# Optimization experiments

Hardware: AMD Instinct MI355X
Metric: run time of the kernel (lower is better)

The kernel has to match this reference:

```python
import jax, jax.numpy as jnp
import numpy as np

B = 16384            # number of subgraphs in the batch
NODES_PER_G = 50     # nodes per subgraph
N = B * NODES_PER_G  # total nodes = 819200
L = 3                # num_gcn_layers
EMB = 32             # emb_dim -> repr dim = (1+L)*EMB = 128
REPR = (1 + L) * EMB
PFEAT, FEAT = 1280, 200
P, D, I = 2000, 10000, 20000
RELS = 2


def setup_inputs() -> dict:
    key = jax.random.key(0)
    ks = jax.random.split(key, 16)
    node_repr = jax.random.normal(ks[0], (N, REPR), jnp.float32)
    profeat = jax.random.normal(ks[1], (P, PFEAT), jnp.float32)
    drugfeat = jax.random.normal(ks[2], (D, FEAT), jnp.float32)
    s1p = 1.0 / np.sqrt(PFEAT); s2 = 1.0 / np.sqrt(EMB); s1 = 1.0 / np.sqrt(FEAT)
    W1p = jax.random.normal(ks[3], (PFEAT, EMB), jnp.float32) * s1p
    b1p = jnp.zeros((EMB,), jnp.float32)
    W2p = jax.random.normal(ks[4], (EMB, EMB), jnp.float32) * s2
    b2p = jnp.zeros((EMB,), jnp.float32)
    W1 = jax.random.normal(ks[5], (FEAT, EMB), jnp.float32) * s1
    b1 = jnp.zeros((EMB,), jnp.float32)
    W2 = jax.random.normal(ks[6], (EMB, EMB), jnp.float32) * s2
    b2 = jnp.zeros((EMB,), jnp.float32)
    fc_in = 3 * REPR + 2 * EMB  # 448
    fc_W = jax.random.normal(ks[7], (fc_in, RELS), jnp.float32) / np.sqrt(fc_in)
    fc_b = jnp.zeros((RELS,), jnp.float32)
    # batched-graph structure: contiguous blocks of NODES_PER_G nodes per graph
    graph_ids = (jnp.arange(N, dtype=jnp.int32) // NODES_PER_G).astype(jnp.int32)
    # exactly one head (id==1) and one tail (id==2) node per graph -> their indices
    head_ids = (jnp.arange(B, dtype=jnp.int32) * NODES_PER_G)
    tail_ids = head_ids + 1
    node_idx = jax.random.randint(ks[8], (N,), 0, I, jnp.int32)
    proind = jax.random.randint(ks[9], (I,), 0, P, jnp.int32)
    drugind = jax.random.randint(ks[10], (I,), 0, D, jnp.int32)
    return dict(node_repr=node_repr, profeat=profeat, drugfeat=drugfeat,
                W1p=W1p, b1p=b1p, W2p=W2p, b2p=b2p,
                W1=W1, b1=b1, W2=W2, b2=b2, fc_W=fc_W, fc_b=fc_b,
                graph_ids=graph_ids, head_ids=head_ids, tail_ids=tail_ids,
                node_idx=node_idx, proind=proind, drugind=drugind)


def reference(node_repr, profeat, drugfeat, W1p, b1p, W2p, b2p,
              W1, b1, W2, b2, fc_W, fc_b,
              graph_ids, head_ids, tail_ids, node_idx, proind, drugind):
    # mean_nodes(g, 'repr'): per-graph mean pooling of node reprs
    sums = jax.ops.segment_sum(node_repr, graph_ids, num_segments=B)      # [B, REPR]
    cnts = jax.ops.segment_sum(jnp.ones((node_repr.shape[0],), node_repr.dtype),
                               graph_ids, num_segments=B)                # [B]
    g_out = sums / cnts[:, None]
    # head/tail embedding gathers (id==1 / id==2 nodes)
    head_embs = node_repr[head_ids]                                       # [B, REPR]
    tail_embs = node_repr[tail_ids]                                       # [B, REPR]
    # nested table lookups: profeat[proind[idx[head]]], drugfeat[drugind[idx[tail]]]
    head_feat = profeat[proind[node_idx[head_ids]]]                       # [B, PFEAT]
    tail_feat = drugfeat[drugind[node_idx[tail_ids]]]                     # [B, FEAT]
    # small fuse MLPs (dropout is identity in eval)
    fuse1 = jax.nn.relu(head_feat @ W1p + b1p) @ W2p + b2p                # [B, EMB]
    fuse2 = jax.nn.relu(tail_feat @ W1 + b1) @ W2 + b2                    # [B, EMB]
    g_rep = jnp.concatenate([g_out, head_embs, tail_embs, fuse1, fuse2], axis=1)
    return g_rep @ fc_W + fc_b                                            # [B, RELS]
```

## Files before the change

### kernel.cpp

```cpp
#include <hip/hip_runtime.h>
#include <hip/hip_bf16.h>

#define B_GRAPHS 16384
#define NODES_PER_G 50
#define REPR 128
#define PFEAT 1280
#define FEAT 200
#define EMB 32
#define P_ROWS 2000
#define D_ROWS 10000

#define NPF (P_ROWS / 8)
#define NDF (D_ROWS / 8)
#define NFUSE (NPF + NDF)
#define NPOOL (B_GRAPHS / 8)
#define NTOT (NPOOL + NFUSE)


__global__ __launch_bounds__(256) void merged_kernel(
    const float* __restrict__ nr,
    const float* __restrict__ profeat,
    const float* __restrict__ drugfeat,
    const float* __restrict__ W1p,
    const float* __restrict__ b1p,
    const float* __restrict__ W2p,
    const float* __restrict__ W1,
    const float* __restrict__ b1,
    const float* __restrict__ W2,
    const float* __restrict__ fcW,
    const float* __restrict__ b2p,
    const float* __restrict__ b2,
    float*       __restrict__ f1out,
    float*       __restrict__ f2out,
    float*       __restrict__ out)
{
    const int grp  = threadIdx.x >> 5;
    const int lane = threadIdx.x & 31;
    const int bid  = blockIdx.x;

    const int Fb  = (int)(((long)bid * NFUSE) / NTOT);
    const int Fb1 = (int)(((long)(bid + 1) * NFUSE) / NTOT);

    if (Fb1 == Fb) {
        const int g = (bid - Fb) * 8 + grp;
        const float4* nr4 = (const float4*)nr;
        const long base4 = (long)g * (NODES_PER_G * REPR / 4);

        float4 head4 = nr4[base4 + 0 * 32 + lane];
        float4 tail4 = nr4[base4 + 1 * 32 + lane];
        float4 s0, s1;
        s0.x = s0.y = s0.z = s0.w = 0.f;
        s1.x = s1.y = s1.z = s1.w = 0.f;
        #pragma unroll 8
        for (int i = 2; i < NODES_PER_G; i += 2) {
            float4 fa = nr4[base4 + i * 32 + lane];
            float4 fb = nr4[base4 + (i + 1) * 32 + lane];
            s0.x += fa.x; s0.y += fa.y; s0.z += fa.z; s0.w += fa.w;
            s1.x += fb.x; s1.y += fb.y; s1.z += fb.z; s1.w += fb.w;
        }
        float4 pool;
        pool.x = head4.x + tail4.x + s0.x + s1.x;
        pool.y = head4.y + tail4.y + s0.y + s1.y;
        pool.z = head4.z + tail4.z + s0.z + s1.z;
        pool.w = head4.w + tail4.w + s0.w + s1.w;

        const float4* fcW4 = (const float4*)fcW;
        float4 wg0 = fcW4[lane * 2 + 0],       wg1 = fcW4[lane * 2 + 1];
        float4 wh0 = fcW4[64 + lane * 2 + 0],  wh1 = fcW4[64 + lane * 2 + 1];
        float4 wt0 = fcW4[128 + lane * 2 + 0], wt1 = fcW4[128 + lane * 2 + 1];

        const float inv50 = 1.0f / (float)NODES_PER_G;
        float p0 = inv50 * (pool.x * wg0.x + pool.y * wg0.z + pool.z * wg1.x + pool.w * wg1.z)
                 + head4.x * wh0.x + head4.y * wh0.z + head4.z * wh1.x + head4.w * wh1.z
                 + tail4.x * wt0.x + tail4.y * wt0.z + tail4.z * wt1.x + tail4.w * wt1.z;
        float p1 = inv50 * (pool.x * wg0.y + pool.y * wg0.w + pool.z * wg1.y + pool.w * wg1.w)
                 + head4.x * wh0.y + head4.y * wh0.w + head4.z * wh1.y + head4.w * wh1.w
                 + tail4.x * wt0.y + tail4.y * wt0.w + tail4.z * wt1.y + tail4.w * wt1.w;

        {
            float2 fw1 = *(const float2*)(fcW + (384 + lane) * 2);
            float2 fw2 = *(const float2*)(fcW + (416 + lane) * 2);
            float bb1 = b2p[lane], bb2 = b2[lane];
            p0 = fmaf(bb1, fw1.x, fmaf(bb2, fw2.x, p0));
            p1 = fmaf(bb1, fw1.y, fmaf(bb2, fw2.y, p1));
        }

        for (int m = 16; m >= 1; m >>= 1) {
            p0 += __shfl_xor(p0, m, 32);
            p1 += __shfl_xor(p1, m, 32);
        }
        if (lane == 0) {
            out[g * 2 + 0] = p0;
            out[g * 2 + 1] = p1;
        }
    } else if (Fb < NPF) {
        const int p = Fb * 8 + grp;
        float m0 = 0.f, m1 = 0.f;
        #pragma unroll
        for (int k = 0; k < 32; ++k) {
            float w = W2p[lane * 32 + k];
            float2 fw = *(const float2*)(fcW + (384 + k) * 2);
            m0 = fmaf(w, fw.x, m0);
            m1 = fmaf(w, fw.y, m1);
        }
        const float4* pf4 = (const float4*)(profeat + (long)p * PFEAT);
        float a0 = 0.f, a1 = 0.f, a2 = 0.f, a3 = 0.f;
        #pragma unroll 4
        for (int q = 0; q < PFEAT / 4; q += 4) {
            float4 f0 = pf4[q], f1 = pf4[q + 1], f2 = pf4[q + 2], f3 = pf4[q + 3];
            int k = q * 4;
            a0 = fmaf(f0.x, W1p[(k + 0) * 32 + lane], a0);
            a0 = fmaf(f0.y, W1p[(k + 1) * 32 + lane], a0);
            a0 = fmaf(f0.z, W1p[(k + 2) * 32 + lane], a0);
            a0 = fmaf(f0.w, W1p[(k + 3) * 32 + lane], a0);
            a1 = fmaf(f1.x, W1p[(k + 4) * 32 + lane], a1);
            a1 = fmaf(f1.y, W1p[(k + 5) * 32 + lane], a1);
            a1 = fmaf(f1.z, W1p[(k + 6) * 32 + lane], a1);
            a1 = fmaf(f1.w, W1p[(k + 7) * 32 + lane], a1);
            a2 = fmaf(f2.x, W1p[(k + 8) * 32 + lane], a2);
            a2 = fmaf(f2.y, W1p[(k + 9) * 32 + lane], a2);
            a2 = fmaf(f2.z, W1p[(k + 10) * 32 + lane], a2);
            a2 = fmaf(f2.w, W1p[(k + 11) * 32 + lane], a2);
            a3 = fmaf(f3.x, W1p[(k + 12) * 32 + lane], a3);
            a3 = fmaf(f3.y, W1p[(k + 13) * 32 + lane], a3);
            a3 = fmaf(f3.z, W1p[(k + 14) * 32 + lane], a3);
            a3 = fmaf(f3.w, W1p[(k + 15) * 32 + lane], a3);
        }
        float h = fmaxf((a0 + a1) + (a2 + a3) + b1p[lane], 0.f);
        float p0 = h * m0, p1 = h * m1;
        for (int m = 16; m >= 1; m >>= 1) {
            p0 += __shfl_xor(p0, m, 32);
            p1 += __shfl_xor(p1, m, 32);
        }
        if (lane == 0) {
            f1out[p * 2 + 0] = p0;
            f1out[p * 2 + 1] = p1;
        }
    } else {
        const int d = (Fb - NPF) * 8 + grp;
        float m0 = 0.f, m1 = 0.f;
        #pragma unroll
        for (int k = 0; k < 32; ++k) {
            float w = W2[lane * 32 + k];
            float2 fw = *(const float2*)(fcW + (416 + k) * 2);
            m0 = fmaf(w, fw.x, m0);
            m1 = fmaf(w, fw.y, m1);
        }
        const float4* df4 = (const float4*)(drugfeat + (long)d * FEAT);
        float a0 = 0.f, a1 = 0.f;
        #pragma unroll 5
        for (int q = 0; q < FEAT / 4; q += 2) {
            float4 f0 = df4[q], f1 = df4[q + 1];
            int k = q * 4;
            a0 = fmaf(f0.x, W1[(k + 0) * 32 + lane], a0);
            a0 = fmaf(f0.y, W1[(k + 1) * 32 + lane], a0);
            a0 = fmaf(f0.z, W1[(k + 2) * 32 + lane], a0);
            a0 = fmaf(f0.w, W1[(k + 3) * 32 + lane], a0);
            a1 = fmaf(f1.x, W1[(k + 4) * 32 + lane], a1);
            a1 = fmaf(f1.y, W1[(k + 5) * 32 + lane], a1);
            a1 = fmaf(f1.z, W1[(k + 6) * 32 + lane], a1);
            a1 = fmaf(f1.w, W1[(k + 7) * 32 + lane], a1);
        }
        float h = fmaxf(a0 + a1 + b1[lane], 0.f);
        float p0 = h * m0, p1 = h * m1;
        for (int m = 16; m >= 1; m >>= 1) {
            p0 += __shfl_xor(p0, m, 32);
            p1 += __shfl_xor(p1, m, 32);
        }
        if (lane == 0) {
            f2out[d * 2 + 0] = p0;
            f2out[d * 2 + 1] = p1;
        }
    }
}

__global__ __launch_bounds__(256) void finalize_kernel(
    const int*   __restrict__ head_ids,
    const int*   __restrict__ tail_ids,
    const int*   __restrict__ node_idx,
    const int*   __restrict__ proind,
    const int*   __restrict__ drugind,
    const float* __restrict__ f1out,
    const float* __restrict__ f2out,
    const float* __restrict__ fcb,
    float*       __restrict__ out)
{
    const int g = blockIdx.x * 256 + threadIdx.x;
    if (g >= B_GRAPHS) return;
    const int prow = proind[node_idx[head_ids[g]]];
    const int drow = drugind[node_idx[tail_ids[g]]];
    const float2 f1v = *(const float2*)(f1out + prow * 2);
    const float2 f2v = *(const float2*)(f2out + drow * 2);
    float2 o = *(float2*)(out + g * 2);
    o.x += f1v.x + f2v.x + fcb[0];
    o.y += f1v.y + f2v.y + fcb[1];
    *(float2*)(out + g * 2) = o;
}

extern "C" void kernel_launch(void* const* d_in, const int* in_sizes, int n_in,
                              void* d_out, int out_size, void* d_ws, size_t ws_size,
                              hipStream_t stream) {
    const float* node_repr = (const float*)d_in[0];
    const float* profeat   = (const float*)d_in[1];
    const float* drugfeat  = (const float*)d_in[2];
    const float* W1p       = (const float*)d_in[3];
    const float* b1p       = (const float*)d_in[4];
    const float* W2p       = (const float*)d_in[5];
    const float* b2p       = (const float*)d_in[6];
    const float* W1        = (const float*)d_in[7];
    const float* b1        = (const float*)d_in[8];
    const float* W2        = (const float*)d_in[9];
    const float* b2        = (const float*)d_in[10];
    const float* fc_W      = (const float*)d_in[11];
    const float* fc_b      = (const float*)d_in[12];
    const int* head_ids    = (const int*)d_in[14];
    const int* tail_ids    = (const int*)d_in[15];
    const int* node_idx    = (const int*)d_in[16];
    const int* proind      = (const int*)d_in[17];
    const int* drugind     = (const int*)d_in[18];

    float* f1out = (float*)d_ws;
    float* f2out = (float*)d_ws + 2 * P_ROWS;
    float* out   = (float*)d_out;

    hipLaunchKernelGGL(merged_kernel, dim3(NTOT), dim3(256), 0, stream,
                       node_repr, profeat, drugfeat, W1p, b1p, W2p, W1, b1, W2,
                       fc_W, b2p, b2, f1out, f2out, out);

    hipLaunchKernelGGL(finalize_kernel, dim3(B_GRAPHS / 256), dim3(256), 0, stream,
                       head_ids, tail_ids, node_idx, proind, drugind,
                       f1out, f2out, fc_b, out);
}
```

Before: 107.3 us.

## Use one full 64-lane wavefront per graph in pooling branch

The pooling branch now assigns a whole 64-lane wavefront to each graph instead of a 32-lane half. Each lane reads two node rows per step, so the 50-node sum takes 25 loads split across four accumulators rather than 48 sequential loads over two. Head and tail rows are split across the two halves of the wavefront, and the bias terms go with them. Launch bounds now request 8 blocks per CU, which caps register use. The trade-off is twice as many pooling blocks and a longer shuffle reduction.

After: 133.3 us. 1.24x slower.

```diff
diff --git a/kernel.cpp b/kernel.cpp
--- a/kernel.cpp
+++ b/kernel.cpp
@@ -13,11 +13,11 @@
 #define NPF (P_ROWS / 8)
 #define NDF (D_ROWS / 8)
 #define NFUSE (NPF + NDF)
-#define NPOOL (B_GRAPHS / 8)
+#define NPOOL (B_GRAPHS / 4)
 #define NTOT (NPOOL + NFUSE)
 
 
-__global__ __launch_bounds__(256) void merged_kernel(
+__global__ __launch_bounds__(256, 8) void merged_kernel(
     const float* __restrict__ nr,
     const float* __restrict__ profeat,
     const float* __restrict__ drugfeat,
@@ -34,66 +34,78 @@
     float*       __restrict__ f2out,
     float*       __restrict__ out)
 {
-    const int grp  = threadIdx.x >> 5;
-    const int lane = threadIdx.x & 31;
     const int bid  = blockIdx.x;
-
     const int Fb  = (int)(((long)bid * NFUSE) / NTOT);
     const int Fb1 = (int)(((long)(bid + 1) * NFUSE) / NTOT);
 
     if (Fb1 == Fb) {
-        const int g = (bid - Fb) * 8 + grp;
+        const int wid = threadIdx.x >> 6;
+        const int l   = threadIdx.x & 63;
+        const int col = l & 31;
+        const int g   = (bid - Fb) * 4 + wid;
+
         const float4* nr4 = (const float4*)nr;
         const long base4 = (long)g * (NODES_PER_G * REPR / 4);
 
-        float4 head4 = nr4[base4 + 0 * 32 + lane];
-        float4 tail4 = nr4[base4 + 1 * 32 + lane];
-        float4 s0, s1;
-        s0.x = s0.y = s0.z = s0.w = 0.f;
-        s1.x = s1.y = s1.z = s1.w = 0.f;
-        #pragma unroll 8
-        for (int i = 2; i < NODES_PER_G; i += 2) {
-            float4 fa = nr4[base4 + i * 32 + lane];
-            float4 fb = nr4[base4 + (i + 1) * 32 + lane];
-            s0.x += fa.x; s0.y += fa.y; s0.z += fa.z; s0.w += fa.w;
-            s1.x += fb.x; s1.y += fb.y; s1.z += fb.z; s1.w += fb.w;
+        float4 sp = nr4[base4 + l];
+        float4 a0, a1, a2, a3;
+        a0 = sp;
+        a1.x = a1.y = a1.z = a1.w = 0.f;
+        a2.x = a2.y = a2.z = a2.w = 0.f;
+        a3.x = a3.y = a3.z = a3.w = 0.f;
+        #pragma unroll
+        for (int it = 1; it <= 24; it += 4) {
+            float4 f0 = nr4[base4 + (it + 0) * 64 + l];
+            float4 f1 = nr4[base4 + (it + 1) * 64 + l];
+            float4 f2 = nr4[base4 + (it + 2) * 64 + l];
+            float4 f3 = nr4[base4 + (it + 3) * 64 + l];
+            a0.x += f0.x; a0.y += f0.y; a0.z += f0.z; a0.w += f0.w;
+            a1.x += f1.x; a1.y += f1.y; a1.z += f1.z; a1.w += f1.w;
+            a2.x += f2.x; a2.y += f2.y; a2.z += f2.z; a2.w += f2.w;
+            a3.x += f3.x; a3.y += f3.y; a3.z += f3.z; a3.w += f3.w;
         }
         float4 pool;
-        pool.x = head4.x + tail4.x + s0.x + s1.x;
-        pool.y = head4.y + tail4.y + s0.y + s1.y;
-        pool.z = head4.z + tail4.z + s0.z + s1.z;
-        pool.w = head4.w + tail4.w + s0.w + s1.w;
+        pool.x = (a0.x + a1.x) + (a2.x + a3.x);
+        pool.y = (a0.y + a1.y) + (a2.y + a3.y);
+        pool.z = (a0.z + a1.z) + (a2.z + a3.z);
+        pool.w = (a0.w + a1.w) + (a2.w + a3.w);
 
         const float4* fcW4 = (const float4*)fcW;
-        float4 wg0 = fcW4[lane * 2 + 0],       wg1 = fcW4[lane * 2 + 1];
-        float4 wh0 = fcW4[64 + lane * 2 + 0],  wh1 = fcW4[64 + lane * 2 + 1];
-        float4 wt0 = fcW4[128 + lane * 2 + 0], wt1 = fcW4[128 + lane * 2 + 1];
+        float4 wg0 = fcW4[col * 2 + 0], wg1 = fcW4[col * 2 + 1];
+        float4 wsp0, wsp1;
+        float2 fwb;
+        float bw;
+        if (l < 32) {
+            wsp0 = fcW4[64 + col * 2 + 0];
+            wsp1 = fcW4[64 + col * 2 + 1];
+            fwb  = *(const float2*)(fcW + (384 + col) * 2);
+            bw   = b2p[col];
+        } else {
+            wsp0 = fcW4[128 + col * 2 + 0];
+            wsp1 = fcW4[128 + col * 2 + 1];
+            fwb  = *(const float2*)(fcW + (416 + col) * 2);
+            bw   = b2[col];
+        }
 
         const float inv50 = 1.0f / (float)NODES_PER_G;
         float p0 = inv50 * (pool.x * wg0.x + pool.y * wg0.z + pool.z * wg1.x + pool.w * wg1.z)
-                 + head4.x * wh0.x + head4.y * wh0.z + head4.z * wh1.x + head4.w * wh1.z
-                 + tail4.x * wt0.x + tail4.y * wt0.z + tail4.z * wt1.x + tail4.w * wt1.z;
+                 + sp.x * wsp0.x + sp.y * wsp0.z + sp.z * wsp1.x + sp.w * wsp1.z
+                 + bw * fwb.x;
         float p1 = inv50 * (pool.x * wg0.y + pool.y * wg0.w + pool.z * wg1.y + pool.w * wg1.w)
-                 + head4.x * wh0.y + head4.y * wh0.w + head4.z * wh1.y + head4.w * wh1.w
-                 + tail4.x * wt0.y + tail4.y * wt0.w + tail4.z * wt1.y + tail4.w * wt1.w;
-
-        {
-            float2 fw1 = *(const float2*)(fcW + (384 + lane) * 2);
-            float2 fw2 = *(const float2*)(fcW + (416 + lane) * 2);
-            float bb1 = b2p[lane], bb2 = b2[lane];
-            p0 = fmaf(bb1, fw1.x, fmaf(bb2, fw2.x, p0));
-            p1 = fmaf(bb1, fw1.y, fmaf(bb2, fw2.y, p1));
-        }
-
-        for (int m = 16; m >= 1; m >>= 1) {
-            p0 += __shfl_xor(p0, m, 32);
-            p1 += __shfl_xor(p1, m, 32);
-        }
-        if (lane == 0) {
+                 + sp.x * wsp0.y + sp.y * wsp0.w + sp.z * wsp1.y + sp.w * wsp1.w
+                 + bw * fwb.y;
+
+        for (int m = 32; m >= 1; m >>= 1) {
+            p0 += __shfl_xor(p0, m, 64);
+            p1 += __shfl_xor(p1, m, 64);
+        }
+        if (l == 0) {
             out[g * 2 + 0] = p0;
             out[g * 2 + 1] = p1;
         }
     } else if (Fb < NPF) {
+        const int grp  = threadIdx.x >> 5;
+        const int lane = threadIdx.x & 31;
         const int p = Fb * 8 + grp;
         float m0 = 0.f, m1 = 0.f;
         #pragma unroll
@@ -137,6 +149,8 @@
             f1out[p * 2 + 1] = p1;
         }
     } else {
+        const int grp  = threadIdx.x >> 5;
+        const int lane = threadIdx.x & 31;
         const int d = (Fb - NPF) * 8 + grp;
         float m0 = 0.f, m1 = 0.f;
         #pragma unroll
```

## Pool each graph with a full 256-thread block using shared-memory reduction

Applied to the files above, without the earlier changes.

Each pooling block now handles a single graph instead of eight. All 256 threads load the graph's contiguous 25.6KB with coalesced float4 reads (six or seven per thread), then reduce through shared memory, and one 32-lane group finishes the fc projection. This aims to expose more memory-level parallelism per wave and shorten the serial accumulation chain. In exchange it launches eight times as many pooling blocks and adds a __syncthreads and a shared-memory reduction step.

New measurement: 119.2 us. 1.11x slower.

```diff
diff --git a/kernel.cpp b/kernel.cpp
--- a/kernel.cpp
+++ b/kernel.cpp
@@ -13,7 +13,7 @@
 #define NPF (P_ROWS / 8)
 #define NDF (D_ROWS / 8)
 #define NFUSE (NPF + NDF)
-#define NPOOL (B_GRAPHS / 8)
+#define NPOOL (B_GRAPHS)
 #define NTOT (NPOOL + NFUSE)
 
 
@@ -34,66 +34,85 @@
     float*       __restrict__ f2out,
     float*       __restrict__ out)
 {
-    const int grp  = threadIdx.x >> 5;
-    const int lane = threadIdx.x & 31;
-    const int bid  = blockIdx.x;
-
+    __shared__ float4 sm[256];
+    __shared__ float4 sht[64];
+
+    const int bid = blockIdx.x;
     const int Fb  = (int)(((long)bid * NFUSE) / NTOT);
     const int Fb1 = (int)(((long)(bid + 1) * NFUSE) / NTOT);
 
     if (Fb1 == Fb) {
-        const int g = (bid - Fb) * 8 + grp;
+        const int t = threadIdx.x;
+        const int g = bid - Fb;
         const float4* nr4 = (const float4*)nr;
         const long base4 = (long)g * (NODES_PER_G * REPR / 4);
 
-        float4 head4 = nr4[base4 + 0 * 32 + lane];
-        float4 tail4 = nr4[base4 + 1 * 32 + lane];
-        float4 s0, s1;
-        s0.x = s0.y = s0.z = s0.w = 0.f;
-        s1.x = s1.y = s1.z = s1.w = 0.f;
-        #pragma unroll 8
-        for (int i = 2; i < NODES_PER_G; i += 2) {
-            float4 fa = nr4[base4 + i * 32 + lane];
-            float4 fb = nr4[base4 + (i + 1) * 32 + lane];
-            s0.x += fa.x; s0.y += fa.y; s0.z += fa.z; s0.w += fa.w;
-            s1.x += fb.x; s1.y += fb.y; s1.z += fb.z; s1.w += fb.w;
-        }
-        float4 pool;
-        pool.x = head4.x + tail4.x + s0.x + s1.x;
-        pool.y = head4.y + tail4.y + s0.y + s1.y;
-        pool.z = head4.z + tail4.z + s0.z + s1.z;
-        pool.w = head4.w + tail4.w + s0.w + s1.w;
-
-        const float4* fcW4 = (const float4*)fcW;
-        float4 wg0 = fcW4[lane * 2 + 0],       wg1 = fcW4[lane * 2 + 1];
-        float4 wh0 = fcW4[64 + lane * 2 + 0],  wh1 = fcW4[64 + lane * 2 + 1];
-        float4 wt0 = fcW4[128 + lane * 2 + 0], wt1 = fcW4[128 + lane * 2 + 1];
-
-        const float inv50 = 1.0f / (float)NODES_PER_G;
-        float p0 = inv50 * (pool.x * wg0.x + pool.y * wg0.z + pool.z * wg1.x + pool.w * wg1.z)
-                 + head4.x * wh0.x + head4.y * wh0.z + head4.z * wh1.x + head4.w * wh1.z
-                 + tail4.x * wt0.x + tail4.y * wt0.z + tail4.z * wt1.x + tail4.w * wt1.z;
-        float p1 = inv50 * (pool.x * wg0.y + pool.y * wg0.w + pool.z * wg1.y + pool.w * wg1.w)
-                 + head4.x * wh0.y + head4.y * wh0.w + head4.z * wh1.y + head4.w * wh1.w
-                 + tail4.x * wt0.y + tail4.y * wt0.w + tail4.z * wt1.y + tail4.w * wt1.w;
-
-        {
-            float2 fw1 = *(const float2*)(fcW + (384 + lane) * 2);
-            float2 fw2 = *(const float2*)(fcW + (416 + lane) * 2);
-            float bb1 = b2p[lane], bb2 = b2[lane];
-            p0 = fmaf(bb1, fw1.x, fmaf(bb2, fw2.x, p0));
-            p1 = fmaf(bb1, fw1.y, fmaf(bb2, fw2.y, p1));
-        }
-
-        for (int m = 16; m >= 1; m >>= 1) {
-            p0 += __shfl_xor(p0, m, 32);
-            p1 += __shfl_xor(p1, m, 32);
-        }
-        if (lane == 0) {
-            out[g * 2 + 0] = p0;
-            out[g * 2 + 1] = p1;
+        float4 f0 = nr4[base4 + 0 * 256 + t];
+        float4 f1 = nr4[base4 + 1 * 256 + t];
+        float4 f2 = nr4[base4 + 2 * 256 + t];
+        float4 f3 = nr4[base4 + 3 * 256 + t];
+        float4 f4 = nr4[base4 + 4 * 256 + t];
+        float4 f5 = nr4[base4 + 5 * 256 + t];
+        float4 ft;
+        if (t < 64) {
+            ft = nr4[base4 + 1536 + t];
+        } else {
+            ft.x = ft.y = ft.z = ft.w = 0.f;
+        }
+
+        if (t < 64) sht[t] = f0;
+
+        float4 acc;
+        acc.x = ((f0.x + f1.x) + (f2.x + f3.x)) + ((f4.x + f5.x) + ft.x);
+        acc.y = ((f0.y + f1.y) + (f2.y + f3.y)) + ((f4.y + f5.y) + ft.y);
+        acc.z = ((f0.z + f1.z) + (f2.z + f3.z)) + ((f4.z + f5.z) + ft.z);
+        acc.w = ((f0.w + f1.w) + (f2.w + f3.w)) + ((f4.w + f5.w) + ft.w);
+        sm[t] = acc;
+        __syncthreads();
+
+        if (t < 32) {
+            float4 pool = sm[t];
+            #pragma unroll
+            for (int j = 1; j < 8; ++j) {
+                float4 v = sm[t + 32 * j];
+                pool.x += v.x; pool.y += v.y; pool.z += v.z; pool.w += v.w;
+            }
+            float4 head4 = sht[t];
+            float4 tail4 = sht[32 + t];
+
+            const float4* fcW4 = (const float4*)fcW;
+            float4 wg0 = fcW4[t * 2 + 0],       wg1 = fcW4[t * 2 + 1];
+            float4 wh0 = fcW4[64 + t * 2 + 0],  wh1 = fcW4[64 + t * 2 + 1];
+            float4 wt0 = fcW4[128 + t * 2 + 0], wt1 = fcW4[128 + t * 2 + 1];
+
+            const float inv50 = 1.0f / (float)NODES_PER_G;
+            float p0 = inv50 * (pool.x * wg0.x + pool.y * wg0.z + pool.z * wg1.x + pool.w * wg1.z)
+                     + head4.x * wh0.x + head4.y * wh0.z + head4.z * wh1.x + head4.w * wh1.z
+                     + tail4.x * wt0.x + tail4.y * wt0.z + tail4.z * wt1.x + tail4.w * wt1.z;
+            float p1 = inv50 * (pool.x * wg0.y + pool.y * wg0.w + pool.z * wg1.y + pool.w * wg1.w)
+                     + head4.x * wh0.y + head4.y * wh0.w + head4.z * wh1.y + head4.w * wh1.w
+                     + tail4.x * wt0.y + tail4.y * wt0.w + tail4.z * wt1.y + tail4.w * wt1.w;
+
+            {
+                float2 fw1 = *(const float2*)(fcW + (384 + t) * 2);
+                float2 fw2 = *(const float2*)(fcW + (416 + t) * 2);
+                float bb1 = b2p[t], bb2 = b2[t];
+                p0 = fmaf(bb1, fw1.x, fmaf(bb2, fw2.x, p0));
+                p1 = fmaf(bb1, fw1.y, fmaf(bb2, fw2.y, p1));
+            }
+
+            for (int m = 16; m >= 1; m >>= 1) {
+                p0 += __shfl_xor(p0, m, 32);
+                p1 += __shfl_xor(p1, m, 32);
+            }
+            if (t == 0) {
+                out[g * 2 + 0] = p0;
+                out[g * 2 + 1] = p1;
+            }
         }
     } else if (Fb < NPF) {
+        const int grp  = threadIdx.x >> 5;
+        const int lane = threadIdx.x & 31;
         const int p = Fb * 8 + grp;
         float m0 = 0.f, m1 = 0.f;
         #pragma unroll
@@ -137,6 +156,8 @@
             f1out[p * 2 + 1] = p1;
         }
     } else {
+        const int grp  = threadIdx.x >> 5;
+        const int lane = threadIdx.x & 31;
         const int d = (Fb - NPF) * 8 + grp;
         float m0 = 0.f, m1 = 0.f;
         #pragma unroll
```
